# Kernel optimization log

Measured on AMD Instinct MI355X. Metric: run time of the kernel, lower is better.

The kernel has to match this reference:

```python
import jax, jax.numpy as jnp
import numpy as np

B, IN_SHAPE, EXP_SHAPE, HID, NB_CLASSES = 64, 10000, 53, 1500, 2048


def setup_inputs() -> dict:
    key = jax.random.key(0)
    ks = jax.random.split(key, 8)
    gos = jax.random.uniform(ks[0], (B, IN_SHAPE), dtype=jnp.float32)
    exp_x = jax.random.uniform(ks[1], (B, EXP_SHAPE), dtype=jnp.float32)
    # FlatModel params (torch Linear: y = x @ W.T + b; store pre-transposed)
    W1 = jax.random.normal(ks[2], (IN_SHAPE, HID), dtype=jnp.float32) * (1.0 / np.sqrt(IN_SHAPE))
    b1 = jnp.zeros((HID,), dtype=jnp.float32)
    W2 = jax.random.normal(ks[3], (HID + EXP_SHAPE, NB_CLASSES), dtype=jnp.float32) * (1.0 / np.sqrt(HID + EXP_SHAPE))
    b2 = jnp.zeros((NB_CLASSES,), dtype=jnp.float32)
    # HPO adjacency (non-trainable buffer in the original; values in [0,1))
    hpo_matrix = jax.random.uniform(ks[4], (NB_CLASSES, NB_CLASSES), dtype=jnp.float32)
    return {"gos": gos, "exp_x": exp_x, "W1": W1, "b1": b1, "W2": W2, "b2": b2, "hpo_matrix": hpo_matrix}


def reference(gos, exp_x, W1, b1, W2, b2, hpo_matrix):
    # FlatModel (eval mode: dropout is identity). torch F.gelu default = exact erf gelu.
    h = jax.nn.gelu(gos @ W1 + b1, approximate=False)          # (B, HID)
    x = jnp.concatenate([h, exp_x], axis=1)                     # (B, HID+EXP)
    flat = jax.nn.sigmoid(x @ W2 + b2)                          # (B, C)
    # HPOLayer + permute + MaxPool1d(C): out[b,j] = max_i flat[b,j] * M[i,j]
    out = jnp.max(flat[:, None, :] * hpo_matrix[None, :, :], axis=1)  # (B, C)
    return out
```

## Files before the change

### kernel.cpp

```cpp
#include <hip/hip_runtime.h>
#include <math.h>

#define B64 64
#define IN_SH 10000
#define EXP_SH 53
#define HID 1500
#define NPAD1 1536
#define NBC 2048
#define K2 1553
#define KS1 40
#define KST1 8
#define KS2 13
#define KST2 4
#define CMCH 32
#define LDSF 2080

using short8  = __attribute__((ext_vector_type(8))) short;
using floatx4 = __attribute__((ext_vector_type(4))) float;
using uintx4  = __attribute__((ext_vector_type(4))) unsigned int;

__device__ __forceinline__ unsigned short f2bf(float f) {
    unsigned u = __float_as_uint(f);
    u += 0x7fffu + ((u >> 16) & 1u);
    return (unsigned short)(u >> 16);
}


__global__ __launch_bounds__(256) void prep_k(const float* __restrict__ g,
                                              unsigned short* __restrict__ gosBf,
                                              const float* __restrict__ M,
                                              float* __restrict__ cm,
                                              float* __restrict__ accz) {
    int bi = blockIdx.x;
    if (bi < 320) {
        int t    = bi * 256 + threadIdx.x;
        int lane = t & 63;
        int sgrp = (t >> 6) & 3;
        int step = t >> 8;
        int q    = lane >> 4;
        int l15  = lane & 15;
        int b    = sgrp * 16 + l15;
        int k0   = step * 32 + q * 8;
        const float* p = g + (size_t)b * IN_SH + k0;
        unsigned int o[4];
        #pragma unroll
        for (int i = 0; i < 4; i++) {
            float lo = (k0 + 2 * i     < IN_SH) ? p[2 * i]     : 0.f;
            float hi = (k0 + 2 * i + 1 < IN_SH) ? p[2 * i + 1] : 0.f;
            o[i] = (unsigned)f2bf(lo) | ((unsigned)f2bf(hi) << 16);
        }
        uintx4 v; v.x = o[0]; v.y = o[1]; v.z = o[2]; v.w = o[3];
        *(uintx4*)(gosBf + (size_t)t * 8) = v;
    } else if (bi < 576) {
        int ci = bi - 320;
        int j  = (ci & 7) * 256 + threadIdx.x;
        int i0 = (ci >> 3) * 64;
        float m = 0.0f;
        #pragma unroll 16
        for (int i = i0; i < i0 + 64; i++)
            m = fmaxf(m, M[(size_t)i * NBC + j]);
        cm[(ci >> 3) * NBC + j] = m;
    } else {
        int t = (bi - 576) * 256 + threadIdx.x;
        floatx4 z = (floatx4){0.f, 0.f, 0.f, 0.f};
        #pragma unroll
        for (int i = 0; i < 28; i++)
            *(floatx4*)(accz + (size_t)(i * 2048 + t) * 4) = z;
    }
}

__device__ __forceinline__ void load_b4(const unsigned short* __restrict__ bf,
                                        int stg, uintx4 bv[4]) {
    #pragma unroll
    for (int s = 0; s < 4; s++)
        bv[s] = *(const uintx4*)(bf + (size_t)(stg * 4 + s) * 512);
}

__device__ __forceinline__ void stage_load(
    const float* __restrict__ W, int kg0, int n0, int N, int K, int ldw,
    int tid, bool fast, float r[2][4])
{
    #pragma unroll
    for (int i = 0; i < 2; i++) {
        int kl = (tid >> 4) + 16 * i;
        int kg = kg0 + kl;
        int n  = n0 + (tid & 15) * 4;
        if (fast) {
            floatx4 v = *(const floatx4*)(W + (size_t)kg * ldw + n);
            r[i][0] = v.x; r[i][1] = v.y; r[i][2] = v.z; r[i][3] = v.w;
        } else {
            #pragma unroll
            for (int j = 0; j < 4; j++)
                r[i][j] = (kg < K && n + j < N) ? W[(size_t)kg * ldw + n + j] : 0.f;
        }
    }
}

__device__ __forceinline__ void stage_write(float* __restrict__ ldsb, int tid,
                                            const float r[2][4]) {
    #pragma unroll
    for (int i = 0; i < 2; i++) {
        int kl  = (tid >> 4) + 16 * i;
        int seg = tid & 15;
        floatx4 v; v.x = r[i][0]; v.y = r[i][1]; v.z = r[i][2]; v.w = r[i][3];
        *(floatx4*)(ldsb + kl * 65 + seg * 4) = v;
    }
}

template<int KSTEPS>
__device__ __forceinline__ void gemm_core(
    const float* __restrict__ W, const unsigned short* __restrict__ Bf,
    float* __restrict__ accbuf, int N, int K, int ldw, int bx, int by, int tid,
    float (*lds)[LDSF])
{
    int w    = tid >> 6;
    int lane = tid & 63;
    int q    = lane >> 4;
    int l15  = lane & 15;
    int n0   = bx * 64;
    int k0   = by * (KSTEPS * 32);
    bool fast = (n0 + 64 <= N) && (k0 + KSTEPS * 32 <= K);

    const unsigned short* bf = Bf + (size_t)(by * KSTEPS * 4) * 512 + (size_t)lane * 8;

    floatx4 acc[4];
    #pragma unroll
    for (int s = 0; s < 4; s++) acc[s] = (floatx4){0.f, 0.f, 0.f, 0.f};

    float r[2][4];
    stage_load(W, k0, n0, N, K, ldw, tid, fast, r);
    stage_write(lds[0], tid, r);

    uintx4 bv[2][4];
    load_b4(bf, 0, bv[0]);
    if (KSTEPS > 1) load_b4(bf, 1, bv[1]);

    #pragma unroll
    for (int st = 0; st < KSTEPS; st++) {
        if (st + 1 < KSTEPS)
            stage_load(W, k0 + (st + 1) * 32, n0, N, K, ldw, tid, fast, r);
        uintx4 bt[4];
        if (st + 2 < KSTEPS) load_b4(bf, st + 2, bt);

        __syncthreads();

        const float* lb = lds[st & 1];
        short8 af;
        #pragma unroll
        for (int j = 0; j < 8; j++)
            af[j] = (short)f2bf(lb[(q * 8 + j) * 65 + 16 * w + l15]);

        const int p = st & 1;
        #pragma unroll
        for (int s = 0; s < 4; s++) {
            short8 bf8 = __builtin_bit_cast(short8, bv[p][s]);
            acc[s] = __builtin_amdgcn_mfma_f32_16x16x32_bf16(af, bf8, acc[s], 0, 0, 0);
        }

        if (st + 1 < KSTEPS)
            stage_write(lds[(st + 1) & 1], tid, r);
        if (st + 2 < KSTEPS) {
            #pragma unroll
            for (int s = 0; s < 4; s++) bv[p][s] = bt[s];
        }
    }

    int nrow = n0 + 16 * w + q * 4;
    #pragma unroll
    for (int s = 0; s < 4; s++) {
        #pragma unroll
        for (int rr = 0; rr < 4; rr++)
            atomicAdd(&accbuf[(size_t)(nrow + rr) * 64 + s * 16 + l15], acc[s][rr]);
    }
}

__global__ __launch_bounds__(256) void gemm1_k(
    const float* __restrict__ W1, const unsigned short* __restrict__ gosBf,
    float* __restrict__ hpre)
{
    __shared__ float lds[2][LDSF];
    gemm_core<KST1>(W1, gosBf, hpre, HID, IN_SH, HID, blockIdx.x, blockIdx.y,
                    threadIdx.x, lds);
}

__global__ __launch_bounds__(256) void gemm2_k(
    const float* __restrict__ W2, const unsigned short* __restrict__ Xf,
    float* __restrict__ logits)
{
    __shared__ float lds[2][LDSF];
    gemm_core<KST2>(W2, Xf, logits, NBC, K2, NBC, blockIdx.x, blockIdx.y,
                    threadIdx.x, lds);
}

__global__ __launch_bounds__(256) void combine1(
    const float* __restrict__ hpre, const float* __restrict__ b1,
    const float* __restrict__ expx, unsigned short* __restrict__ Xf)
{
    int t    = blockIdx.x * 256 + threadIdx.x;
    int lane = t & 63;
    int sgrp = (t >> 6) & 3;
    int step = t >> 8;
    int q    = lane >> 4;
    int l15  = lane & 15;
    int b    = sgrp * 16 + l15;
    int kb   = step * 32 + q * 8;
    unsigned int o[4];
    #pragma unroll
    for (int i = 0; i < 4; i++) {
        unsigned int lohi[2];
        #pragma unroll
        for (int h = 0; h < 2; h++) {
            int n = kb + 2 * i + h;
            float v = 0.f;
            if (n < HID) {
                float s = hpre[(size_t)n * 64 + b] + b1[n];
                v = 0.5f * s * (1.0f + erff(s * 0.70710678118654752f));
            } else if (n < HID + EXP_SH) {
                v = expx[b * EXP_SH + (n - HID)];
            }
            lohi[h] = f2bf(v);
        }
        o[i] = lohi[0] | (lohi[1] << 16);
    }
    uintx4 v; v.x = o[0]; v.y = o[1]; v.z = o[2]; v.w = o[3];
    *(uintx4*)(Xf + (size_t)t * 8) = v;
}

__global__ __launch_bounds__(256) void final_k(
    const float* __restrict__ logits, const float* __restrict__ b2,
    const float* __restrict__ cm, float* __restrict__ out)
{
    int idx = blockIdx.x * 256 + threadIdx.x;
    int b = idx & 63;
    int j = idx >> 6;
    float s = logits[(size_t)j * 64 + b] + b2[j];
    float sig = 1.0f / (1.0f + expf(-s));
    float m = 0.f;
    #pragma unroll
    for (int c = 0; c < CMCH; c++) m = fmaxf(m, cm[c * NBC + j]);
    out[(size_t)b * NBC + j] = sig * m;
}

extern "C" void kernel_launch(void* const* d_in, const int* in_sizes, int n_in,
                              void* d_out, int out_size, void* d_ws, size_t ws_size,
                              hipStream_t stream) {
    const float* gos  = (const float*)d_in[0];
    const float* expx = (const float*)d_in[1];
    const float* W1   = (const float*)d_in[2];
    const float* b1   = (const float*)d_in[3];
    const float* W2   = (const float*)d_in[4];
    const float* b2   = (const float*)d_in[5];
    const float* hpo  = (const float*)d_in[6];
    float* out = (float*)d_out;

    char* ws = (char*)d_ws;
    unsigned short* gosBf = (unsigned short*)ws;
    float* hpre   = (float*)(ws + 1310720);
    float* logits = (float*)(ws + 1310720 + 393216);
    unsigned short* Xf = (unsigned short*)(ws + 1310720 + 393216 + 524288);
    float* cm = (float*)(ws + 1310720 + 393216 + 524288 + 212992);

    prep_k<<<584, 256, 0, stream>>>(gos, gosBf, hpo, cm, hpre);

    gemm1_k<<<dim3(NPAD1 / 64, KS1), 256, 0, stream>>>(W1, gosBf, hpre);

    combine1<<<52, 256, 0, stream>>>(hpre, b1, expx, Xf);

    gemm2_k<<<dim3(NBC / 64, KS2), 256, 0, stream>>>(W2, Xf, logits);

    final_k<<<(B64 * NBC) / 256, 256, 0, stream>>>(logits, b2, cm, out);
}
```

Baseline: 162.4 us.

## Triple-buffer GEMM LDS stages and move column-max into gemm2 launch

The GEMM core now keeps three LDS stages, so the weight load for step st+2 is issued while step st computes, which deepens prefetch and hides more global latency. The hpo column-max reduction moves from the prep kernel into extra blocks of the gemm2 launch. That runs it alongside the second GEMM instead of ahead of the first, shrinking the prep launch. Launch bounds now request 4 waves per EU. The extra LDS buffer raises shared memory per block and may limit occupancy.

Result: slower. 167.2 us (+3.0%).

```diff
diff --git a/kernel.cpp b/kernel.cpp
--- a/kernel.cpp
+++ b/kernel.cpp
@@ -12,6 +12,7 @@
 #define KST1 8
 #define KS2 13
 #define KST2 4
+#define G2BLKS (32 * KS2)
 #define CMCH 32
 #define LDSF 2080
 
@@ -28,8 +29,6 @@
 
 __global__ __launch_bounds__(256) void prep_k(const float* __restrict__ g,
                                               unsigned short* __restrict__ gosBf,
-                                              const float* __restrict__ M,
-                                              float* __restrict__ cm,
                                               float* __restrict__ accz) {
     int bi = blockIdx.x;
     if (bi < 320) {
@@ -51,17 +50,8 @@
         }
         uintx4 v; v.x = o[0]; v.y = o[1]; v.z = o[2]; v.w = o[3];
         *(uintx4*)(gosBf + (size_t)t * 8) = v;
-    } else if (bi < 576) {
-        int ci = bi - 320;
-        int j  = (ci & 7) * 256 + threadIdx.x;
-        int i0 = (ci >> 3) * 64;
-        float m = 0.0f;
-        #pragma unroll 16
-        for (int i = i0; i < i0 + 64; i++)
-            m = fmaxf(m, M[(size_t)i * NBC + j]);
-        cm[(ci >> 3) * NBC + j] = m;
     } else {
-        int t = (bi - 576) * 256 + threadIdx.x;
+        int t = (bi - 320) * 256 + threadIdx.x;
         floatx4 z = (floatx4){0.f, 0.f, 0.f, 0.f};
         #pragma unroll
         for (int i = 0; i < 28; i++)
@@ -130,6 +120,10 @@
     float r[2][4];
     stage_load(W, k0, n0, N, K, ldw, tid, fast, r);
     stage_write(lds[0], tid, r);
+    if (KSTEPS > 1) {
+        stage_load(W, k0 + 32, n0, N, K, ldw, tid, fast, r);
+        stage_write(lds[1], tid, r);
+    }
 
     uintx4 bv[2][4];
     load_b4(bf, 0, bv[0]);
@@ -137,14 +131,15 @@
 
     #pragma unroll
     for (int st = 0; st < KSTEPS; st++) {
-        if (st + 1 < KSTEPS)
-            stage_load(W, k0 + (st + 1) * 32, n0, N, K, ldw, tid, fast, r);
         uintx4 bt[4];
-        if (st + 2 < KSTEPS) load_b4(bf, st + 2, bt);
+        if (st + 2 < KSTEPS) {
+            stage_load(W, k0 + (st + 2) * 32, n0, N, K, ldw, tid, fast, r);
+            load_b4(bf, st + 2, bt);
+        }
 
         __syncthreads();
 
-        const float* lb = lds[st & 1];
+        const float* lb = lds[st % 3];
         short8 af;
         #pragma unroll
         for (int j = 0; j < 8; j++)
@@ -157,9 +152,8 @@
             acc[s] = __builtin_amdgcn_mfma_f32_16x16x32_bf16(af, bf8, acc[s], 0, 0, 0);
         }
 
-        if (st + 1 < KSTEPS)
-            stage_write(lds[(st + 1) & 1], tid, r);
         if (st + 2 < KSTEPS) {
+            stage_write(lds[(st + 2) % 3], tid, r);
             #pragma unroll
             for (int s = 0; s < 4; s++) bv[p][s] = bt[s];
         }
@@ -174,22 +168,34 @@
     }
 }
 
-__global__ __launch_bounds__(256) void gemm1_k(
+__global__ __launch_bounds__(256, 4) void gemm1_k(
     const float* __restrict__ W1, const unsigned short* __restrict__ gosBf,
     float* __restrict__ hpre)
 {
-    __shared__ float lds[2][LDSF];
+    __shared__ float lds[3][LDSF];
     gemm_core<KST1>(W1, gosBf, hpre, HID, IN_SH, HID, blockIdx.x, blockIdx.y,
                     threadIdx.x, lds);
 }
 
-__global__ __launch_bounds__(256) void gemm2_k(
+__global__ __launch_bounds__(256, 4) void gemm2_k(
     const float* __restrict__ W2, const unsigned short* __restrict__ Xf,
-    float* __restrict__ logits)
-{
-    __shared__ float lds[2][LDSF];
-    gemm_core<KST2>(W2, Xf, logits, NBC, K2, NBC, blockIdx.x, blockIdx.y,
-                    threadIdx.x, lds);
+    float* __restrict__ logits, const float* __restrict__ M, float* __restrict__ cm)
+{
+    __shared__ float lds[3][LDSF];
+    int bi = blockIdx.x;
+    if (bi < G2BLKS) {
+        gemm_core<KST2>(W2, Xf, logits, NBC, K2, NBC, bi & 31, bi >> 5,
+                        threadIdx.x, lds);
+    } else {
+        int ci = bi - G2BLKS;
+        int j  = (ci & 7) * 256 + threadIdx.x;
+        int i0 = (ci >> 3) * 64;
+        float m = 0.0f;
+        #pragma unroll 16
+        for (int i = i0; i < i0 + 64; i++)
+            m = fmaxf(m, M[(size_t)i * NBC + j]);
+        cm[(ci >> 3) * NBC + j] = m;
+    }
 }
 
 __global__ __launch_bounds__(256) void combine1(
@@ -260,13 +266,13 @@
     unsigned short* Xf = (unsigned short*)(ws + 1310720 + 393216 + 524288);
     float* cm = (float*)(ws + 1310720 + 393216 + 524288 + 212992);
 
-    prep_k<<<584, 256, 0, stream>>>(gos, gosBf, hpo, cm, hpre);
+    prep_k<<<328, 256, 0, stream>>>(gos, gosBf, hpre);
 
     gemm1_k<<<dim3(NPAD1 / 64, KS1), 256, 0, stream>>>(W1, gosBf, hpre);
 
     combine1<<<52, 256, 0, stream>>>(hpre, b1, expx, Xf);
 
-    gemm2_k<<<dim3(NBC / 64, KS2), 256, 0, stream>>>(W2, Xf, logits);
+    gemm2_k<<<G2BLKS + 256, 256, 0, stream>>>(W2, Xf, logits, hpo, cm);
 
     final_k<<<(B64 * NBC) / 256, 256, 0, stream>>>(logits, b2, cm, out);
 }
```

## Fuse GELU combine and sigmoid-max epilogue into split-K GEMMs via last-block counters

Applied to the files above, without the earlier changes.

Removes the separate combine1 and final_k kernel launches. Each split-K GEMM column tile now keeps an atomic arrival counter, and the last block to finish runs the epilogue: GELU and bf16 packing for gemm1, and sigmoid times the column max for gemm2. The zeroing in prep_k is widened to also clear the counters, and the exp_x tail of Xf is written in prep_k. The change saves two launches and their drain gaps, but it adds threadfence and atomic overhead and serialises the epilogue onto a few blocks.

Measured after the change: 322.9 us. 98.9% more time.

```diff
diff --git a/kernel.cpp b/kernel.cpp
--- a/kernel.cpp
+++ b/kernel.cpp
@@ -26,11 +26,53 @@
 }
 
 
+template<bool AGENTLOAD>
+__device__ __forceinline__ void combine_tuple(
+    int t, const float* __restrict__ hpre, const float* __restrict__ b1,
+    const float* __restrict__ expx, unsigned short* __restrict__ Xf)
+{
+    int lane = t & 63;
+    int sgrp = (t >> 6) & 3;
+    int step = t >> 8;
+    int q    = lane >> 4;
+    int l15  = lane & 15;
+    int b    = sgrp * 16 + l15;
+    int kb   = step * 32 + q * 8;
+    unsigned int o[4];
+    #pragma unroll
+    for (int i = 0; i < 4; i++) {
+        unsigned int lohi[2];
+        #pragma unroll
+        for (int h = 0; h < 2; h++) {
+            int n = kb + 2 * i + h;
+            float v = 0.f;
+            if (n < HID) {
+                float s;
+                if (AGENTLOAD)
+                    s = __hip_atomic_load(&hpre[(size_t)n * 64 + b],
+                                          __ATOMIC_RELAXED, __HIP_MEMORY_SCOPE_AGENT);
+                else
+                    s = hpre[(size_t)n * 64 + b];
+                s += b1[n];
+                v = 0.5f * s * (1.0f + erff(s * 0.70710678118654752f));
+            } else if (n < HID + EXP_SH) {
+                v = expx[b * EXP_SH + (n - HID)];
+            }
+            lohi[h] = f2bf(v);
+        }
+        o[i] = lohi[0] | (lohi[1] << 16);
+    }
+    uintx4 v; v.x = o[0]; v.y = o[1]; v.z = o[2]; v.w = o[3];
+    *(uintx4*)(Xf + (size_t)t * 8) = v;
+}
+
 __global__ __launch_bounds__(256) void prep_k(const float* __restrict__ g,
                                               unsigned short* __restrict__ gosBf,
                                               const float* __restrict__ M,
                                               float* __restrict__ cm,
-                                              float* __restrict__ accz) {
+                                              float* __restrict__ accz,
+                                              const float* __restrict__ expx,
+                                              unsigned short* __restrict__ Xf) {
     int bi = blockIdx.x;
     if (bi < 320) {
         int t    = bi * 256 + threadIdx.x;
@@ -60,12 +102,17 @@
         for (int i = i0; i < i0 + 64; i++)
             m = fmaxf(m, M[(size_t)i * NBC + j]);
         cm[(ci >> 3) * NBC + j] = m;
-    } else {
+    } else if (bi < 585) {
         int t = (bi - 576) * 256 + threadIdx.x;
         floatx4 z = (floatx4){0.f, 0.f, 0.f, 0.f};
         #pragma unroll
-        for (int i = 0; i < 28; i++)
-            *(floatx4*)(accz + (size_t)(i * 2048 + t) * 4) = z;
+        for (int i = 0; i < 25; i++)
+            *(floatx4*)(accz + (size_t)(i * 2304 + t) * 4) = z;
+    } else {
+        #pragma unroll
+        for (int it = 0; it < 4; it++)
+            combine_tuple<false>(12288 + it * 256 + (int)threadIdx.x,
+                                 nullptr, nullptr, expx, Xf);
     }
 }
 
@@ -174,71 +221,63 @@
     }
 }
 
+__device__ __forceinline__ bool last_done(int* cnt, int bx, int target, int* flag) {
+    __threadfence();
+    if (threadIdx.x == 0) {
+        int old = __hip_atomic_fetch_add(&cnt[bx], 1, __ATOMIC_ACQ_REL,
+                                         __HIP_MEMORY_SCOPE_AGENT);
+        *flag = (old == target - 1);
+    }
+    __syncthreads();
+    return *flag != 0;
+}
+
 __global__ __launch_bounds__(256) void gemm1_k(
     const float* __restrict__ W1, const unsigned short* __restrict__ gosBf,
-    float* __restrict__ hpre)
+    float* __restrict__ hpre, const float* __restrict__ b1,
+    const float* __restrict__ expx, unsigned short* __restrict__ Xf,
+    int* __restrict__ c1)
 {
     __shared__ float lds[2][LDSF];
-    gemm_core<KST1>(W1, gosBf, hpre, HID, IN_SH, HID, blockIdx.x, blockIdx.y,
+    __shared__ int flag;
+    int bx = blockIdx.x;
+    gemm_core<KST1>(W1, gosBf, hpre, HID, IN_SH, HID, bx, blockIdx.y,
                     threadIdx.x, lds);
+    if (last_done(c1, bx, KS1, &flag)) {
+        #pragma unroll
+        for (int it = 0; it < 2; it++)
+            combine_tuple<true>(bx * 512 + it * 256 + (int)threadIdx.x,
+                                hpre, b1, expx, Xf);
+    }
 }
 
 __global__ __launch_bounds__(256) void gemm2_k(
     const float* __restrict__ W2, const unsigned short* __restrict__ Xf,
-    float* __restrict__ logits)
+    float* __restrict__ logits, const float* __restrict__ b2,
+    const float* __restrict__ cm, float* __restrict__ out,
+    int* __restrict__ c2)
 {
     __shared__ float lds[2][LDSF];
-    gemm_core<KST2>(W2, Xf, logits, NBC, K2, NBC, blockIdx.x, blockIdx.y,
+    __shared__ int flag;
+    int bx = blockIdx.x;
+    gemm_core<KST2>(W2, Xf, logits, NBC, K2, NBC, bx, blockIdx.y,
                     threadIdx.x, lds);
-}
-
-__global__ __launch_bounds__(256) void combine1(
-    const float* __restrict__ hpre, const float* __restrict__ b1,
-    const float* __restrict__ expx, unsigned short* __restrict__ Xf)
-{
-    int t    = blockIdx.x * 256 + threadIdx.x;
-    int lane = t & 63;
-    int sgrp = (t >> 6) & 3;
-    int step = t >> 8;
-    int q    = lane >> 4;
-    int l15  = lane & 15;
-    int b    = sgrp * 16 + l15;
-    int kb   = step * 32 + q * 8;
-    unsigned int o[4];
-    #pragma unroll
-    for (int i = 0; i < 4; i++) {
-        unsigned int lohi[2];
-        #pragma unroll
-        for (int h = 0; h < 2; h++) {
-            int n = kb + 2 * i + h;
-            float v = 0.f;
-            if (n < HID) {
-                float s = hpre[(size_t)n * 64 + b] + b1[n];
-                v = 0.5f * s * (1.0f + erff(s * 0.70710678118654752f));
-            } else if (n < HID + EXP_SH) {
-                v = expx[b * EXP_SH + (n - HID)];
-            }
-            lohi[h] = f2bf(v);
-        }
-        o[i] = lohi[0] | (lohi[1] << 16);
-    }
-    uintx4 v; v.x = o[0]; v.y = o[1]; v.z = o[2]; v.w = o[3];
-    *(uintx4*)(Xf + (size_t)t * 8) = v;
-}
-
-__global__ __launch_bounds__(256) void final_k(
-    const float* __restrict__ logits, const float* __restrict__ b2,
-    const float* __restrict__ cm, float* __restrict__ out)
-{
-    int idx = blockIdx.x * 256 + threadIdx.x;
-    int b = idx & 63;
-    int j = idx >> 6;
-    float s = logits[(size_t)j * 64 + b] + b2[j];
-    float sig = 1.0f / (1.0f + expf(-s));
-    float m = 0.f;
-    #pragma unroll
-    for (int c = 0; c < CMCH; c++) m = fmaxf(m, cm[c * NBC + j]);
-    out[(size_t)b * NBC + j] = sig * m;
+    if (last_done(c2, bx, KS2, &flag)) {
+        int j  = bx * 64 + ((int)threadIdx.x & 63);
+        int b0 = ((int)threadIdx.x >> 6) * 16;
+        float m = 0.f;
+        #pragma unroll
+        for (int c = 0; c < CMCH; c++) m = fmaxf(m, cm[c * NBC + j]);
+        float bj = b2[j];
+        #pragma unroll
+        for (int i = 0; i < 16; i++) {
+            int b = b0 + i;
+            float s = __hip_atomic_load(&logits[(size_t)j * 64 + b],
+                                        __ATOMIC_RELAXED, __HIP_MEMORY_SCOPE_AGENT) + bj;
+            float sig = 1.0f / (1.0f + expf(-s));
+            out[(size_t)b * NBC + j] = sig * m;
+        }
+    }
 }
 
 extern "C" void kernel_launch(void* const* d_in, const int* in_sizes, int n_in,
@@ -257,16 +296,14 @@
     unsigned short* gosBf = (unsigned short*)ws;
     float* hpre   = (float*)(ws + 1310720);
     float* logits = (float*)(ws + 1310720 + 393216);
-    unsigned short* Xf = (unsigned short*)(ws + 1310720 + 393216 + 524288);
-    float* cm = (float*)(ws + 1310720 + 393216 + 524288 + 212992);
-
-    prep_k<<<584, 256, 0, stream>>>(gos, gosBf, hpo, cm, hpre);
-
-    gemm1_k<<<dim3(NPAD1 / 64, KS1), 256, 0, stream>>>(W1, gosBf, hpre);
-
-    combine1<<<52, 256, 0, stream>>>(hpre, b1, expx, Xf);
-
-    gemm2_k<<<dim3(NBC / 64, KS2), 256, 0, stream>>>(W2, Xf, logits);
-
-    final_k<<<(B64 * NBC) / 256, 256, 0, stream>>>(logits, b2, cm, out);
-}
+    int*   c1     = (int*)  (ws + 2228224);
+    int*   c2     = c1 + 32;
+    unsigned short* Xf = (unsigned short*)(ws + 2232320);
+    float* cm     = (float*)(ws + 2445312);
+
+    prep_k<<<586, 256, 0, stream>>>(gos, gosBf, hpo, cm, hpre, expx, Xf);
+
+    gemm1_k<<<dim3(NPAD1 / 64, KS1), 256, 0, stream>>>(W1, gosBf, hpre, b1, expx, Xf, c1);
+
+    gemm2_k<<<dim3(NBC / 64, KS2), 256, 0, stream>>>(W2, Xf, logits, b2, cm, out, c2);
+}
```
